# Kernel optimization log

Measured on AMD Instinct MI355X. Metric: run time of the kernel, lower is better.

Reference implementation:

```python
import jax, jax.numpy as jnp
import numpy as np
from jax import lax

B, K, Z, C, H, W = 32, 7, 64, 3, 64, 64
G = H + 6  # decoder grid for 'small' variant
ITERS = 3
SCALE = Z ** -0.5
EPS = 1e-8


def _pe(h, w):
    # matches SlotAttention.create_positional_embedding: shape [w, h, 4]
    ww = jnp.linspace(0.0, 1.0, w)
    hh = jnp.linspace(0.0, 1.0, h)
    a = jnp.broadcast_to((1.0 - ww)[:, None], (w, h))  # dist_right
    b = jnp.broadcast_to(ww[:, None], (w, h))          # dist_left
    c = jnp.broadcast_to(hh[None, :], (w, h))          # dist_top
    d = jnp.broadcast_to((1.0 - hh)[None, :], (w, h))  # dist_bottom
    return jnp.stack([a, b, c, d], -1)


def _ln(x, g, b):
    m = x.mean(-1, keepdims=True)
    v = ((x - m) ** 2).mean(-1, keepdims=True)
    return (x - m) * lax.rsqrt(v + 1e-5) * g + b


def _conv(x, w, b, p):
    y = lax.conv_general_dilated(x, w, (1, 1), [(p, p), (p, p)],
                                 dimension_numbers=('NCHW', 'OIHW', 'NCHW'))
    return y + b[None, :, None, None]


def setup_inputs() -> dict:
    key = jax.random.key(0)
    ks = iter(jax.random.split(key, 64))
    nrm = lambda shape, s=0.05: jax.random.normal(next(ks), shape, jnp.float32) * s
    d = {}
    d['inputs'] = jax.random.normal(next(ks), (B, C, H, W), jnp.float32)
    d['noise'] = jax.random.normal(next(ks), (B * K, Z), jnp.float32)
    d['enc_pos_w'] = nrm((4, 64)); d['enc_pos_b'] = jnp.zeros(64, jnp.float32)
    d['ec1_w'] = nrm((64, 3, 5, 5)); d['ec1_b'] = jnp.zeros(64, jnp.float32)
    d['ec2_w'] = nrm((64, 64, 5, 5)); d['ec2_b'] = jnp.zeros(64, jnp.float32)
    d['ec3_w'] = nrm((64, 64, 5, 5)); d['ec3_b'] = jnp.zeros(64, jnp.float32)
    d['ec4_w'] = nrm((64, 64, 5, 5)); d['ec4_b'] = jnp.zeros(64, jnp.float32)
    d['ln1_g'] = jnp.ones(64, jnp.float32); d['ln1_b'] = jnp.zeros(64, jnp.float32)
    d['fc1_w'] = nrm((64, 64)); d['fc1_b'] = jnp.zeros(64, jnp.float32)
    d['fc2_w'] = nrm((64, 64)); d['fc2_b'] = jnp.zeros(64, jnp.float32)
    d['lns_g'] = jnp.ones(Z, jnp.float32); d['lns_b'] = jnp.zeros(Z, jnp.float32)
    d['lnf_g'] = jnp.ones(Z, jnp.float32); d['lnf_b'] = jnp.zeros(Z, jnp.float32)
    d['q_w'] = nrm((Z, Z)); d['k_w'] = nrm((64, Z)); d['v_w'] = nrm((64, Z))
    d['mlp1_w'] = nrm((Z, 128)); d['mlp1_b'] = jnp.zeros(128, jnp.float32)
    d['mlp2_w'] = nrm((128, Z)); d['mlp2_b'] = jnp.zeros(Z, jnp.float32)
    d['gru_wih'] = nrm((3 * Z, Z)); d['gru_whh'] = nrm((3 * Z, Z))
    d['gru_bih'] = jnp.zeros(3 * Z, jnp.float32); d['gru_bhh'] = jnp.zeros(3 * Z, jnp.float32)
    d['init_slots'] = jnp.concatenate([jnp.zeros((1, Z), jnp.float32), jnp.ones((1, Z), jnp.float32)], 1)
    d['dec_pos_w'] = nrm((4, Z)); d['dec_pos_b'] = jnp.zeros(Z, jnp.float32)
    d['dc1_w'] = nrm((32, Z, 5, 5)); d['dc1_b'] = jnp.zeros(32, jnp.float32)
    d['dc2_w'] = nrm((32, 32, 5, 5)); d['dc2_b'] = jnp.zeros(32, jnp.float32)
    d['dc3_w'] = nrm((32, 32, 5, 5)); d['dc3_b'] = jnp.zeros(32, jnp.float32)
    d['dc4_w'] = nrm((4, 32, 3, 3)); d['dc4_b'] = jnp.zeros(4, jnp.float32)
    return d


def _forward(inputs, noise, enc_pos_w, enc_pos_b, ec1_w, ec1_b, ec2_w, ec2_b,
             ec3_w, ec3_b, ec4_w, ec4_b, ln1_g, ln1_b, fc1_w, fc1_b, fc2_w, fc2_b,
             lns_g, lns_b, lnf_g, lnf_b, q_w, k_w, v_w, mlp1_w, mlp1_b, mlp2_w,
             mlp2_b, gru_wih, gru_whh, gru_bih, gru_bhh, init_slots, dec_pos_w,
             dec_pos_b, dc1_w, dc1_b, dc2_w, dc2_b, dc3_w, dc3_b, dc4_w, dc4_b):
    # ---- encoder ----
    h = jax.nn.relu(_conv(inputs, ec1_w, ec1_b, 2))
    h = jax.nn.relu(_conv(h, ec2_w, ec2_b, 2))
    h = jax.nn.relu(_conv(h, ec3_w, ec3_b, 2))
    h = jax.nn.relu(_conv(h, ec4_w, ec4_b, 2))
    h = h.transpose(0, 2, 3, 1)                        # [B,H,W,64]
    pe = _pe(H, W) @ enc_pos_w + enc_pos_b             # [W,H,64] (H==W)
    h = h + pe[None]
    feat = h.reshape(B, H * W, 64)
    feat = _ln(feat, ln1_g, ln1_b)
    feat = jax.nn.relu(feat @ fc1_w + fc1_b) @ fc2_w + fc2_b
    k = feat @ k_w                                     # [B,N,Z]
    v = feat @ v_w
    # ---- slot init: Normal(loc, softplus(sp)).rsample() ----
    loc, sp = jnp.split(init_slots, 2, axis=1)
    slots = (loc + jax.nn.softplus(sp) * noise).reshape(B, K, Z)
    # ---- iterative slot attention ----
    for _ in range(ITERS):
        prev = slots
        q = (_ln(prev, lns_g, lns_b) @ q_w) * SCALE
        dots = jnp.einsum('bid,bjd->bij', q, k)        # [B,K,N]
        attn = jax.nn.softmax(dots, axis=1) + EPS      # normalize over slots
        attn = attn / attn.sum(-1, keepdims=True)      # renormalize over keys
        updates = jnp.einsum('bjd,bij->bid', v, attn)  # [B,K,Z]
        # GRU cell (single step), torch gate order r,z,n
        gi = updates.reshape(-1, Z) @ gru_wih.T + gru_bih
        gh = prev.reshape(-1, Z) @ gru_whh.T + gru_bhh
        ir, iz, inn = jnp.split(gi, 3, -1)
        hr, hz, hn = jnp.split(gh, 3, -1)
        r = jax.nn.sigmoid(ir + hr)
        zg = jax.nn.sigmoid(iz + hz)
        n = jnp.tanh(inn + r * hn)
        slots = ((1.0 - zg) * n + zg * prev.reshape(-1, Z)).reshape(B, K, Z)
        slots = slots + (jax.nn.relu(_ln(slots, lnf_g, lnf_b) @ mlp1_w + mlp1_b) @ mlp2_w + mlp2_b)
    # ---- spatial-broadcast decoder ('small') ----
    flat = slots.reshape(B * K, Z)
    zb = jnp.broadcast_to(flat[:, :, None, None], (B * K, Z, G, G))
    pe_d = (_pe(G, G) @ dec_pos_w + dec_pos_b).transpose(2, 0, 1)  # [Z,G,G]
    zb = zb + pe_d[None]
    o = jax.nn.relu(_conv(zb, dc1_w, dc1_b, 1))        # 70->68
    o = jax.nn.relu(_conv(o, dc2_w, dc2_b, 1))         # 68->66
    o = jax.nn.relu(_conv(o, dc3_w, dc3_b, 1))         # 66->64
    o = _conv(o, dc4_w, dc4_b, 1)                      # 64->64, 4ch
    x_loc = jax.nn.sigmoid(o[:, :3]).reshape(B, K, C, H, W)
    mask_logits = o[:, 3].reshape(B, K, 1, H, W)
    mask_logp = jax.nn.log_softmax(mask_logits, axis=1)
    x_orig = (inputs + 1.0) / 2.0
    recon = (x_loc * jnp.exp(mask_logp)).sum(1)
    mse = ((x_orig - recon) ** 2).sum() / B
    return mse, x_loc, mask_logp, slots


def reference(inputs, noise, enc_pos_w, enc_pos_b, ec1_w, ec1_b, ec2_w, ec2_b,
              ec3_w, ec3_b, ec4_w, ec4_b, ln1_g, ln1_b, fc1_w, fc1_b, fc2_w, fc2_b,
              lns_g, lns_b, lnf_g, lnf_b, q_w, k_w, v_w, mlp1_w, mlp1_b, mlp2_w,
              mlp2_b, gru_wih, gru_whh, gru_bih, gru_bhh, init_slots, dec_pos_w,
              dec_pos_b, dc1_w, dc1_b, dc2_w, dc2_b, dc3_w, dc3_b, dc4_w, dc4_b):
    return _forward(inputs, noise, enc_pos_w, enc_pos_b, ec1_w, ec1_b, ec2_w, ec2_b,
                    ec3_w, ec3_b, ec4_w, ec4_b, ln1_g, ln1_b, fc1_w, fc1_b, fc2_w, fc2_b,
                    lns_g, lns_b, lnf_g, lnf_b, q_w, k_w, v_w, mlp1_w, mlp1_b, mlp2_w,
                    mlp2_b, gru_wih, gru_whh, gru_bih, gru_bhh, init_slots, dec_pos_w,
                    dec_pos_b, dc1_w, dc1_b, dc2_w, dc2_b, dc3_w, dc3_b, dc4_w, dc4_b)
```

## Files before the change

kernel.cpp:

```cpp
#include <hip/hip_runtime.h>
#include <math.h>

typedef short bf16x8 __attribute__((ext_vector_type(8)));
typedef float f32x4 __attribute__((ext_vector_type(4)));

#define WS_B0   0u
#define WS_B1   4194304u
#define WS_K    8388608u
#define WS_V    16777216u
#define WS_ATTN 25165824u
#define WS_PART 26083328u
#define WS_SLOT 26327040u
#define WS_ROW  26341376u
#define SCALE_ 0.125f

#define OFF_PEB   0u
#define OFF_WCLS  160000u
#define OFF_S     180000u
#define OFF_ZB    250000u

__device__ __forceinline__ float wave_sum(float v) {
#pragma unroll
    for (int m = 32; m >= 1; m >>= 1) v += __shfl_xor(v, m, 64);
    return v;
}
__device__ __forceinline__ unsigned short f2bf(float f) {
    unsigned u = __float_as_uint(f);
    u = u + 0x7fffu + ((u >> 16) & 1u);
    return (unsigned short)(u >> 16);
}
__device__ __forceinline__ float bf2f(unsigned short h) {
    return __uint_as_float(((unsigned)h) << 16);
}

__global__ __launch_bounds__(256) void pack_weights(
    const float* __restrict__ w, unsigned short* __restrict__ wp,
    int CIN, int COUT_STORE, int KS, int NT, int total)
{
    int t = blockIdx.x * 256 + threadIdx.x;
    if (t >= total) return;
    int lane = t & 63;
    int nt = (t >> 6) % NT;
    int ch = t / (64 * NT);
    int CPT = CIN / 32;
    int cic = ch % CPT;
    int tap = ch / CPT;
    int ky = tap / KS, kx = tap % KS;
    int co = nt * 16 + (lane & 15);
    int k0 = cic * 32 + (lane >> 4) * 8;
    unsigned short v[8];
#pragma unroll
    for (int j = 0; j < 8; ++j) {
        int ci = k0 + j;
        float f = (co < COUT_STORE) ? w[((size_t)(co * CIN + ci) * KS + ky) * KS + kx] : 0.f;
        v[j] = f2bf(f);
    }
    *(uint4*)(wp + (size_t)t * 8) = *(uint4*)v;
}

__global__ __launch_bounds__(256) void pack_weights3(
    const float* __restrict__ w0, const float* __restrict__ w1,
    const float* __restrict__ w2, unsigned short* __restrict__ wp)
{
    int t = blockIdx.x * 256 + threadIdx.x;
    if (t >= 38400) return;
    int which = t / 12800;
    int tt = t % 12800;
    const float* w = (which == 0) ? w0 : ((which == 1) ? w1 : w2);
    unsigned short* dst = wp + (size_t)which * 102400;
    int lane = tt & 63;
    int nt = (tt >> 6) & 3;
    int ch = tt >> 8;
    int cic = ch & 1;
    int tap = ch >> 1;
    int ky = tap / 5, kx = tap % 5;
    int co = nt * 16 + (lane & 15);
    int k0 = cic * 32 + (lane >> 4) * 8;
    unsigned short v[8];
#pragma unroll
    for (int j = 0; j < 8; ++j) {
        int ci = k0 + j;
        v[j] = f2bf(w[((size_t)(co * 64 + ci) * 5 + ky) * 5 + kx]);
    }
    *(uint4*)(dst + (size_t)tt * 8) = *(uint4*)v;
}

__global__ __launch_bounds__(256) void pack_fc4(
    const float* __restrict__ w0, const float* __restrict__ w1,
    const float* __restrict__ w2, const float* __restrict__ w3,
    unsigned short* __restrict__ wp)
{
    int t = blockIdx.x * 256 + threadIdx.x;
    if (t >= 2048) return;
    int which = t / 512;
    int tt = t % 512;
    const float* w = (which == 0) ? w0 : ((which == 1) ? w1 : ((which == 2) ? w2 : w3));
    unsigned short* dst = wp + (size_t)which * 4096;
    int lane = tt & 63;
    int nt = (tt >> 6) & 3;
    int ck = tt >> 8;
    int n = nt * 16 + (lane & 15);
    int k0 = ck * 32 + (lane >> 4) * 8;
    unsigned short v[8];
#pragma unroll
    for (int j = 0; j < 8; ++j) v[j] = f2bf(w[(size_t)(k0 + j) * 64 + n]);
    *(uint4*)(dst + (size_t)tt * 8) = *(uint4*)v;
}

template<int CIN, int NTT, int NTU, int KS, int PAD, int NSTORE, int RELU, int OUTF32>
__global__ __launch_bounds__(256) void conv_mfma(
    const unsigned short* __restrict__ in, const unsigned short* __restrict__ wpack,
    const float* __restrict__ bias, void* __restrict__ outv,
    int Hin, int Win, int Hout, int Wout, int tilesX, int tilesY)
{
    constexpr int TS = 16, TH = TS + KS - 1;
    constexpr int CPT = CIN / 32;
    constexpr int G8 = CIN / 8;
    constexpr int CS = NTT / NTU;
    __shared__ __align__(16) unsigned short tile[TH][TH][CIN];
    const int tpb = tilesX * tilesY;
    const int blk = blockIdx.x;
    const int n = blk / (tpb * CS);
    const int rem = blk % (tpb * CS);
    const int t = rem / CS;
    const int cog = rem % CS;
    const int ntb = cog * NTU;
    const int ty0 = (t / tilesX) * TS, tx0 = (t % tilesX) * TS;
    const int tid = threadIdx.x;

    const unsigned short* inb = in + (size_t)n * Hin * Win * CIN;
    for (int idx = tid; idx < TH * TH * G8; idx += 256) {
        const int r = idx / (TH * G8);
        const int p = idx % (TH * G8);
        const int c = p / G8;
        const int chunk = p % G8;
        const int g = (chunk - c) & (G8 - 1);
        int iy = ty0 - PAD + r, ix = tx0 - PAD + c;
        uint4 vv = make_uint4(0, 0, 0, 0);
        if (iy >= 0 && iy < Hin && ix >= 0 && ix < Win)
            vv = *(const uint4*)(inb + ((size_t)iy * Win + ix) * CIN + g * 8);
        *(uint4*)&tile[r][c][chunk * 8] = vv;
    }
    __syncthreads();

    const int wv = tid >> 6, lane = tid & 63;
    const int q = lane >> 4, m = lane & 15;
    const int row0 = wv * 4;
    f32x4 acc[4][NTU];
#pragma unroll
    for (int mt = 0; mt < 4; ++mt)
#pragma unroll
        for (int nt = 0; nt < NTU; ++nt) acc[mt][nt] = (f32x4){0.f, 0.f, 0.f, 0.f};

#pragma unroll
    for (int cic = 0; cic < CPT; ++cic) {
#pragma unroll
        for (int kx = 0; kx < KS; ++kx) {
            bf16x8 B[KS][NTU];
#pragma unroll
            for (int ky = 0; ky < KS; ++ky)
#pragma unroll
                for (int nt = 0; nt < NTU; ++nt)
                    B[ky][nt] = *(const bf16x8*)(wpack +
                        ((size_t)(((ky * KS + kx) * CPT + cic) * NTT + ntb + nt) * 64 + lane) * 8);
            const int cbase = m + kx;
            const int slot = (cic * 32 + q * 8 + cbase * 8) % CIN;
#pragma unroll
            for (int ir = 0; ir < KS + 3; ++ir) {
                bf16x8 afr = *(const bf16x8*)&tile[row0 + ir][cbase][slot];
#pragma unroll
                for (int ky = 0; ky < KS; ++ky) {
                    const int mt = ir - ky;
                    if (mt < 0 || mt > 3) continue;
#pragma unroll
                    for (int nt = 0; nt < NTU; ++nt)
                        acc[mt][nt] = __builtin_amdgcn_mfma_f32_16x16x32_bf16(afr, B[ky][nt], acc[mt][nt], 0, 0, 0);
                }
            }
        }
    }

#pragma unroll
    for (int nt = 0; nt < NTU; ++nt) {
        const int co = (ntb + nt) * 16 + m;
        const float bv = (co < NSTORE) ? bias[co] : 0.f;
#pragma unroll
        for (int mt = 0; mt < 4; ++mt) {
            const int oy = ty0 + wv * 4 + mt;
#pragma unroll
            for (int j = 0; j < 4; ++j) {
                const int ox = tx0 + q * 4 + j;
                if (oy < Hout && ox < Wout && co < NSTORE) {
                    float v = acc[mt][nt][j] + bv;
                    if (RELU) v = fmaxf(v, 0.f);
                    size_t o = (((size_t)n * Hout + oy) * Wout + ox) * NSTORE + co;
                    if (OUTF32) ((float*)outv)[o] = v;
                    else ((unsigned short*)outv)[o] = f2bf(v);
                }
            }
        }
    }
}

__global__ __launch_bounds__(256) void pe_synth(
    const float* __restrict__ dpw, const float* __restrict__ dpb,
    unsigned short* __restrict__ peb, float* __restrict__ zbias)
{
    const int tid = threadIdx.x;
    if (blockIdx.x == 0 && tid < 32) zbias[tid] = 0.f;
    const int pix = blockIdx.x * 256 + tid;
    if (pix >= 4900) return;
    const int iy = pix / 70, ix = pix % 70;
    const float fy = iy * (1.f / 69.f), fx = ix * (1.f / 69.f);
    unsigned short v[64];
#pragma unroll
    for (int ci = 0; ci < 64; ++ci) {
        float p = (1.f - fy) * dpw[ci] + fy * dpw[64 + ci]
                + fx * dpw[128 + ci] + (1.f - fx) * dpw[192 + ci] + dpb[ci];
        v[ci] = f2bf(p);
    }
    uint4* ob = (uint4*)(peb + (size_t)pix * 64);
#pragma unroll
    for (int i = 0; i < 8; ++i) ob[i] = ((uint4*)v)[i];
}

__global__ __launch_bounds__(256) void wcls_build(
    const float* __restrict__ w, float* __restrict__ wcls)
{
    int idx = blockIdx.x * 256 + threadIdx.x;
    if (idx >= 9 * 32 * 64) return;
    int cls = idx / (32 * 64);
    int co = (idx / 64) % 32;
    int ci = idx % 64;
    int rc = cls / 3, cc = cls % 3;
    int ky0 = (rc == 0) ? 1 : 0, ky1 = (rc == 2) ? 3 : 4;
    int kx0 = (cc == 0) ? 1 : 0, kx1 = (cc == 2) ? 3 : 4;
    float s = 0.f;
    const float* wb = w + (size_t)(co * 64 + ci) * 25;
    for (int ky = ky0; ky <= ky1; ++ky)
        for (int kx = kx0; kx <= kx1; ++kx)
            s += wb[ky * 5 + kx];
    wcls[idx] = s;
}

__global__ __launch_bounds__(256) void slot_s(
    const float* __restrict__ slots, const float* __restrict__ wcls,
    float* __restrict__ S)
{
    int idx = blockIdx.x * 256 + threadIdx.x;
    if (idx >= 224 * 9 * 32) return;
    int n = idx / (9 * 32);
    int cls = (idx / 32) % 9;
    int co = idx % 32;
    const float* sl = slots + n * 64;
    const float* wc = wcls + (size_t)(cls * 32 + co) * 64;
    float s = 0.f;
#pragma unroll
    for (int ci = 0; ci < 64; ++ci) s = fmaf(sl[ci], wc[ci], s);
    S[idx] = s;
}

__global__ __launch_bounds__(256) void dc1_assemble(
    const float* __restrict__ P, const float* __restrict__ S,
    const float* __restrict__ bias, int n0,
    unsigned short* __restrict__ out)
{
    const int gid = blockIdx.x * 256 + threadIdx.x;
    const int nl = gid / 4624;
    const int pix = gid % 4624;
    const int oy = pix / 68, ox = pix % 68;
    const int rc = (oy == 0) ? 0 : ((oy == 67) ? 2 : 1);
    const int cc = (ox == 0) ? 0 : ((ox == 67) ? 2 : 1);
    const float* Sp = S + ((size_t)(n0 + nl) * 9 + (rc * 3 + cc)) * 32;
    const float* Pp = P + (size_t)pix * 32;
    unsigned short v[32];
#pragma unroll
    for (int co = 0; co < 32; ++co)
        v[co] = f2bf(fmaxf(bias[co] + Pp[co] + Sp[co], 0.f));
    uint4* ob = (uint4*)(out + ((size_t)nl * 4624 + pix) * 32);
#pragma unroll
    for (int i = 0; i < 4; ++i) ob[i] = ((uint4*)v)[i];
}

__global__ __launch_bounds__(256) void conv_ec1(
    const float* __restrict__ in, const float* __restrict__ wts,
    const float* __restrict__ bias, unsigned short* __restrict__ out)
{
    __shared__ float tile[3][20][21];
    const int blk = blockIdx.x;
    const int n = blk >> 6;
    const int sub = blk & 63;
    const int t = sub >> 2;
    const int cog = sub & 3;
    const int ty0 = (t >> 2) * 16, tx0 = (t & 3) * 16;
    const int tid = threadIdx.x;
    for (int idx = tid; idx < 1200; idx += 256) {
        int ci = idx / 400, rc = idx % 400;
        int r = rc / 20, c = rc % 20;
        int gy = ty0 + r - 2, gx = tx0 + c - 2;
        float v = 0.f;
        if (gy >= 0 && gy < 64 && gx >= 0 && gx < 64)
            v = in[((size_t)n * 3 + ci) * 4096 + gy * 64 + gx];
        tile[ci][r][c] = v;
    }
    __syncthreads();
    const int lx = tid & 15, ly = tid >> 4;
    float acc[16];
#pragma unroll
    for (int co = 0; co < 16; ++co) acc[co] = bias[cog * 16 + co];
    for (int ci = 0; ci < 3; ++ci) {
        float val[25];
#pragma unroll
        for (int ky = 0; ky < 5; ++ky)
#pragma unroll
            for (int kx = 0; kx < 5; ++kx) val[ky * 5 + kx] = tile[ci][ly + ky][lx + kx];
#pragma unroll
        for (int co = 0; co < 16; ++co) {
            const float* wc = wts + (size_t)((cog * 16 + co) * 3 + ci) * 25;
            float a = acc[co];
#pragma unroll
            for (int tt = 0; tt < 25; ++tt) a = fmaf(val[tt], wc[tt], a);
            acc[co] = a;
        }
    }
    unsigned short tmp[16];
#pragma unroll
    for (int co = 0; co < 16; ++co) tmp[co] = f2bf(fmaxf(acc[co], 0.f));
    uint4* ob = (uint4*)(out + (((size_t)n * 64 + ty0 + ly) * 64 + tx0 + lx) * 64 + cog * 16);
    ob[0] = ((uint4*)tmp)[0];
    ob[1] = ((uint4*)tmp)[1];
}

__global__ __launch_bounds__(256) void encoder_tail_mfma(
    const unsigned short* __restrict__ h4,
    const float* __restrict__ epw, const float* __restrict__ epb,
    const float* __restrict__ ln1g, const float* __restrict__ ln1b,
    const unsigned short* __restrict__ pfc1, const float* __restrict__ fc1b,
    const unsigned short* __restrict__ pfc2, const float* __restrict__ fc2b,
    const unsigned short* __restrict__ pkw, const unsigned short* __restrict__ pvw,
    unsigned short* __restrict__ kout, unsigned short* __restrict__ vout)
{
    __shared__ __align__(16) unsigned short X[64][72];
    const int b = blockIdx.x >> 6;
    const int y = blockIdx.x & 63;
    const int tid = threadIdx.x;

    {
        const int p = tid >> 2, sub = tid & 3;
        const unsigned short* hp = h4 + ((((size_t)b * 64 + y) * 64 + p) * 64) + sub * 16;
        unsigned short raw[16];
        *(uint4*)(raw)     = *(const uint4*)hp;
        *(uint4*)(raw + 8) = *(const uint4*)(hp + 8);
        const float fy = y * (1.f / 63.f), fx = p * (1.f / 63.f);
        float f[16];
        float s1 = 0.f, s2 = 0.f;
#pragma unroll
        for (int j = 0; j < 16; ++j) {
            int ch = sub * 16 + j;
            float pe = (1.f - fy) * epw[ch] + fy * epw[64 + ch]
                     + fx * epw[128 + ch] + (1.f - fx) * epw[192 + ch] + epb[ch];
            float v = bf2f(raw[j]) + pe;
            f[j] = v;
            s1 += v;
            s2 += v * v;
        }
        s1 += __shfl_xor(s1, 1, 64); s1 += __shfl_xor(s1, 2, 64);
        s2 += __shfl_xor(s2, 1, 64); s2 += __shfl_xor(s2, 2, 64);
        const float m = s1 * (1.f / 64.f);
        const float var = s2 * (1.f / 64.f) - m * m;
        const float inv = rsqrtf(var + 1e-5f);
        unsigned short xb[16];
#pragma unroll
        for (int j = 0; j < 16; ++j) {
            int ch = sub * 16 + j;
            xb[j] = f2bf((f[j] - m) * inv * ln1g[ch] + ln1b[ch]);
        }
        *(uint4*)&X[p][sub * 16]     = ((uint4*)xb)[0];
        *(uint4*)&X[p][sub * 16 + 8] = ((uint4*)xb)[1];
    }
    __syncthreads();

    const int w = tid >> 6, lane = tid & 63;
    const int q = lane >> 4, m_ = lane & 15;
    const int row0 = w * 16;

    {
        f32x4 a1[4];
#pragma unroll
        for (int nt = 0; nt < 4; ++nt) a1[nt] = (f32x4){0.f, 0.f, 0.f, 0.f};
#pragma unroll
        for (int ck = 0; ck < 2; ++ck) {
            bf16x8 afr = *(const bf16x8*)&X[row0 + m_][ck * 32 + q * 8];
#pragma unroll
            for (int nt = 0; nt < 4; ++nt) {
                bf16x8 bfr = *(const bf16x8*)(pfc1 + ((size_t)((ck * 4 + nt) * 64 + lane)) * 8);
                a1[nt] = __builtin_amdgcn_mfma_f32_16x16x32_bf16(afr, bfr, a1[nt], 0, 0, 0);
            }
        }
        __syncthreads();
#pragma unroll
        for (int nt = 0; nt < 4; ++nt) {
            const float bb = fc1b[nt * 16 + m_];
#pragma unroll
            for (int reg = 0; reg < 4; ++reg)
                X[row0 + q * 4 + reg][nt * 16 + m_] = f2bf(fmaxf(a1[nt][reg] + bb, 0.f));
        }
    }
    __syncthreads();

    {
        f32x4 a2[4];
#pragma unroll
        for (int nt = 0; nt < 4; ++nt) a2[nt] = (f32x4){0.f, 0.f, 0.f, 0.f};
#pragma unroll
        for (int ck = 0; ck < 2; ++ck) {
            bf16x8 afr = *(const bf16x8*)&X[row0 + m_][ck * 32 + q * 8];
#pragma unroll
            for (int nt = 0; nt < 4; ++nt) {
                bf16x8 bfr = *(const bf16x8*)(pfc2 + ((size_t)((ck * 4 + nt) * 64 + lane)) * 8);
                a2[nt] = __builtin_amdgcn_mfma_f32_16x16x32_bf16(afr, bfr, a2[nt], 0, 0, 0);
            }
        }
        __syncthreads();
#pragma unroll
        for (int nt = 0; nt < 4; ++nt) {
            const float bb = fc2b[nt * 16 + m_];
#pragma unroll
            for (int reg = 0; reg < 4; ++reg)
                X[row0 + q * 4 + reg][nt * 16 + m_] = f2bf(a2[nt][reg] + bb);
        }
    }
    __syncthreads();

    {
        f32x4 ak[4], av[4];
#pragma unroll
        for (int nt = 0; nt < 4; ++nt) {
            ak[nt] = (f32x4){0.f, 0.f, 0.f, 0.f};
            av[nt] = (f32x4){0.f, 0.f, 0.f, 0.f};
        }
#pragma unroll
        for (int ck = 0; ck < 2; ++ck) {
            bf16x8 afr = *(const bf16x8*)&X[row0 + m_][ck * 32 + q * 8];
#pragma unroll
            for (int nt = 0; nt < 4; ++nt) {
                bf16x8 bk = *(const bf16x8*)(pkw + ((size_t)((ck * 4 + nt) * 64 + lane)) * 8);
                bf16x8 bv = *(const bf16x8*)(pvw + ((size_t)((ck * 4 + nt) * 64 + lane)) * 8);
                ak[nt] = __builtin_amdgcn_mfma_f32_16x16x32_bf16(afr, bk, ak[nt], 0, 0, 0);
                av[nt] = __builtin_amdgcn_mfma_f32_16x16x32_bf16(afr, bv, av[nt], 0, 0, 0);
            }
        }
        const size_t base = ((size_t)b * 4096) + y * 64 + row0;
#pragma unroll
        for (int nt = 0; nt < 4; ++nt) {
            const int ch = nt * 16 + m_;
#pragma unroll
            for (int reg = 0; reg < 4; ++reg) {
                const size_t o = (base + q * 4 + reg) * 64 + ch;
                kout[o] = f2bf(ak[nt][reg]);
                vout[o] = f2bf(av[nt][reg]);
            }
        }
    }
}

__global__ __launch_bounds__(256) void slot_init(
    const float* __restrict__ noise, const float* __restrict__ init_slots,
    float* __restrict__ slots, float* __restrict__ rowsum)
{
    int i = blockIdx.x * 256 + threadIdx.x;
    if (i < 224) rowsum[i] = 0.f;
    if (i < 224 * 64) {
        int z = i & 63;
        float spl = log1pf(expf(init_slots[64 + z]));
        slots[i] = init_slots[z] + spl * noise[i];
    }
}

__global__ __launch_bounds__(256) void attn_fused(
    const unsigned short* __restrict__ kbuf, const unsigned short* __restrict__ vbuf,
    const float* __restrict__ slots,
    const float* __restrict__ lnsg, const float* __restrict__ lnsb,
    const float* __restrict__ qw,
    float* __restrict__ part, float* __restrict__ rowsum)
{
    __shared__ float qs[7][64];
    __shared__ float ash[256][7];
    __shared__ float red7[7][4];
    __shared__ float redv[4][7][64];
    const int b = blockIdx.x >> 4;
    const int js = blockIdx.x & 15;
    const int j0 = js * 256;
    const int tid = threadIdx.x;
    const int lane = tid & 63, wv = tid >> 6;

    for (int i = wv; i < 7; i += 4) {
        float s = slots[(b * 7 + i) * 64 + lane];
        float m = wave_sum(s) * (1.f / 64.f);
        float d = s - m;
        float var = wave_sum(d * d) * (1.f / 64.f);
        float x = d * rsqrtf(var + 1e-5f) * lnsg[lane] + lnsb[lane];
        float qv = 0.f;
        for (int c = 0; c < 64; ++c) qv = fmaf(__shfl(x, c, 64), qw[c * 64 + lane], qv);
        qs[i][lane] = qv * SCALE_;
    }
    __syncthreads();

    {
        const int j = j0 + tid;
        float kr[64];
        const unsigned short* kp = kbuf + (((size_t)b * 4096) + j) * 64;
#pragma unroll
        for (int d8 = 0; d8 < 8; ++d8) {
            uint4 kv = ((const uint4*)kp)[d8];
            const unsigned short* h = (const unsigned short*)&kv;
#pragma unroll
            for (int z = 0; z < 8; ++z) kr[d8 * 8 + z] = bf2f(h[z]);
        }
        float dots[7];
#pragma unroll
        for (int i = 0; i < 7; ++i) {
            float a = 0.f;
#pragma unroll
            for (int d = 0; d < 64; ++d) a = fmaf(kr[d], qs[i][d], a);
            dots[i] = a;
        }
        float mx = dots[0];
#pragma unroll
        for (int i = 1; i < 7; ++i) mx = fmaxf(mx, dots[i]);
        float sum = 0.f;
#pragma unroll
        for (int i = 0; i < 7; ++i) { dots[i] = expf(dots[i] - mx); sum += dots[i]; }
        const float inv = 1.f / sum;
#pragma unroll
        for (int i = 0; i < 7; ++i) {
            float a = dots[i] * inv + 1e-8f;
            dots[i] = a;
            ash[tid][i] = a;
        }
#pragma unroll
        for (int i = 0; i < 7; ++i) {
            float s = wave_sum(dots[i]);
            if (lane == 0) red7[i][wv] = s;
        }
    }
    __syncthreads();
    if (tid < 7)
        atomicAdd(&rowsum[b * 7 + tid], red7[tid][0] + red7[tid][1] + red7[tid][2] + red7[tid][3]);

    {
        const int d = lane, jc = wv;
        float acc[7];
#pragma unroll
        for (int i = 0; i < 7; ++i) acc[i] = 0.f;
        for (int jl = jc; jl < 256; jl += 4) {
            float av = bf2f(vbuf[(((size_t)b * 4096) + j0 + jl) * 64 + d]);
#pragma unroll
            for (int i = 0; i < 7; ++i)
                acc[i] = fmaf(ash[jl][i], av, acc[i]);
        }
#pragma unroll
        for (int i = 0; i < 7; ++i) redv[jc][i][d] = acc[i];
    }
    __syncthreads();
    if (tid < 7 * 64) {
        int i = tid / 64, dd = tid % 64;
        float s = redv[0][i][dd] + redv[1][i][dd] + redv[2][i][dd] + redv[3][i][dd];
        part[((((size_t)b * 16) + js) * 7 + i) * 64 + dd] = s;
    }
}

__global__ __launch_bounds__(64) void gru_mlp(
    float* __restrict__ slots, const float* __restrict__ part,
    float* __restrict__ rowsum,
    const float* __restrict__ wih, const float* __restrict__ whh,
    const float* __restrict__ bih, const float* __restrict__ bhh,
    const float* __restrict__ lnfg, const float* __restrict__ lnfb,
    const float* __restrict__ m1w, const float* __restrict__ m1b,
    const float* __restrict__ m2w, const float* __restrict__ m2b)
{
    const int n = blockIdx.x;
    const int b = n / 7, i = n % 7;
    const int l = threadIdx.x;
    float upd = 0.f;
    for (int js = 0; js < 16; ++js)
        upd += part[((((size_t)b * 16) + js) * 7 + i) * 64 + l];
    upd /= rowsum[n];
    if (l == 0) rowsum[n] = 0.f;
    const float prev = slots[n * 64 + l];
    float gi0 = bih[l], gi1 = bih[64 + l], gi2 = bih[128 + l];
    float gh0 = bhh[l], gh1 = bhh[64 + l], gh2 = bhh[128 + l];
    for (int c = 0; c < 64; ++c) {
        float u = __shfl(upd, c, 64), p = __shfl(prev, c, 64);
        gi0 = fmaf(u, wih[l * 64 + c], gi0);
        gi1 = fmaf(u, wih[(64 + l) * 64 + c], gi1);
        gi2 = fmaf(u, wih[(128 + l) * 64 + c], gi2);
        gh0 = fmaf(p, whh[l * 64 + c], gh0);
        gh1 = fmaf(p, whh[(64 + l) * 64 + c], gh1);
        gh2 = fmaf(p, whh[(128 + l) * 64 + c], gh2);
    }
    float r  = 1.f / (1.f + expf(-(gi0 + gh0)));
    float zg = 1.f / (1.f + expf(-(gi1 + gh1)));
    float nn = tanhf(gi2 + r * gh2);
    float s = (1.f - zg) * nn + zg * prev;
    float m = wave_sum(s) * (1.f / 64.f);
    float d = s - m;
    float var = wave_sum(d * d) * (1.f / 64.f);
    float x = d * rsqrtf(var + 1e-5f) * lnfg[l] + lnfb[l];
    float h0 = m1b[l], h1 = m1b[64 + l];
    for (int c = 0; c < 64; ++c) {
        float xv = __shfl(x, c, 64);
        h0 = fmaf(xv, m1w[c * 128 + l], h0);
        h1 = fmaf(xv, m1w[c * 128 + 64 + l], h1);
    }
    h0 = fmaxf(h0, 0.f); h1 = fmaxf(h1, 0.f);
    float o = m2b[l];
    for (int c = 0; c < 64; ++c) {
        o = fmaf(__shfl(h0, c, 64), m2w[c * 64 + l], o);
        o = fmaf(__shfl(h1, c, 64), m2w[(64 + c) * 64 + l], o);
    }
    slots[n * 64 + l] = s + o;
}

__global__ __launch_bounds__(256) void finalize_k(
    const float* __restrict__ dc4out, const float* __restrict__ inputs,
    float* __restrict__ out)
{
    const int tid = threadIdx.x;
    const int gp = blockIdx.x * 256 + tid;
    const int b = gp >> 12, p = gp & 4095;
    float4 o4[7];
#pragma unroll
    for (int k = 0; k < 7; ++k)
        o4[k] = ((const float4*)dc4out)[(size_t)(b * 7 + k) * 4096 + p];
    float mx = o4[0].w;
#pragma unroll
    for (int k = 1; k < 7; ++k) mx = fmaxf(mx, o4[k].w);
    float s = 0.f;
#pragma unroll
    for (int k = 0; k < 7; ++k) s += expf(o4[k].w - mx);
    const float lse = mx + logf(s);
    float recon0 = 0.f, recon1 = 0.f, recon2 = 0.f;
    float* xl = out + 1;
    float* ml = out + 2752513;
#pragma unroll
    for (int k = 0; k < 7; ++k) {
        float lp = o4[k].w - lse;
        ml[((size_t)(b * 7 + k)) * 4096 + p] = lp;
        float w = expf(lp);
        float x0 = 1.f / (1.f + expf(-o4[k].x));
        float x1 = 1.f / (1.f + expf(-o4[k].y));
        float x2 = 1.f / (1.f + expf(-o4[k].z));
        xl[(((size_t)(b * 7 + k)) * 3 + 0) * 4096 + p] = x0;
        xl[(((size_t)(b * 7 + k)) * 3 + 1) * 4096 + p] = x1;
        xl[(((size_t)(b * 7 + k)) * 3 + 2) * 4096 + p] = x2;
        recon0 = fmaf(x0, w, recon0);
        recon1 = fmaf(x1, w, recon1);
        recon2 = fmaf(x2, w, recon2);
    }
    float err = 0.f;
    {
        float xo = (inputs[((size_t)b * 3 + 0) * 4096 + p] + 1.f) * 0.5f;
        float dd = xo - recon0; err += dd * dd;
        xo = (inputs[((size_t)b * 3 + 1) * 4096 + p] + 1.f) * 0.5f;
        dd = xo - recon1; err += dd * dd;
        xo = (inputs[((size_t)b * 3 + 2) * 4096 + p] + 1.f) * 0.5f;
        dd = xo - recon2; err += dd * dd;
    }
    float wsum = wave_sum(err);
    __shared__ float red[4];
    const int lane = tid & 63, wv = tid >> 6;
    if (lane == 0) red[wv] = wsum;
    __syncthreads();
    if (tid == 0) atomicAdd(out, (red[0] + red[1] + red[2] + red[3]) * (1.f / 32.f));
}

__global__ __launch_bounds__(256) void copy_slots(const float* __restrict__ slots,
                                                  float* __restrict__ out)
{
    int i = blockIdx.x * 256 + threadIdx.x;
    if (i == 0) out[0] = 0.f;
    if (i < 14336) out[3670017 + i] = slots[i];
}

extern "C" void kernel_launch(void* const* d_in, const int* in_sizes, int n_in,
                              void* d_out, int out_size, void* d_ws, size_t ws_size,
                              hipStream_t stream) {
    (void)in_sizes; (void)n_in; (void)out_size; (void)ws_size;
    const float* inputs = (const float*)d_in[0];
    const float* noise  = (const float*)d_in[1];
    const float* epw  = (const float*)d_in[2];
    const float* epb  = (const float*)d_in[3];
    const float* ec1w = (const float*)d_in[4];
    const float* ec1b = (const float*)d_in[5];
    const float* ec2w = (const float*)d_in[6];
    const float* ec2b = (const float*)d_in[7];
    const float* ec3w = (const float*)d_in[8];
    const float* ec3b = (const float*)d_in[9];
    const float* ec4w = (const float*)d_in[10];
    const float* ec4b = (const float*)d_in[11];
    const float* ln1g = (const float*)d_in[12];
    const float* ln1b = (const float*)d_in[13];
    const float* fc1w = (const float*)d_in[14];
    const float* fc1b = (const float*)d_in[15];
    const float* fc2w = (const float*)d_in[16];
    const float* fc2b = (const float*)d_in[17];
    const float* lnsg = (const float*)d_in[18];
    const float* lnsb = (const float*)d_in[19];
    const float* lnfg = (const float*)d_in[20];
    const float* lnfb = (const float*)d_in[21];
    const float* qw   = (const float*)d_in[22];
    const float* kw   = (const float*)d_in[23];
    const float* vw   = (const float*)d_in[24];
    const float* m1w  = (const float*)d_in[25];
    const float* m1b  = (const float*)d_in[26];
    const float* m2w  = (const float*)d_in[27];
    const float* m2b  = (const float*)d_in[28];
    const float* wih  = (const float*)d_in[29];
    const float* whh  = (const float*)d_in[30];
    const float* bih  = (const float*)d_in[31];
    const float* bhh  = (const float*)d_in[32];
    const float* init_slots = (const float*)d_in[33];
    const float* dpw  = (const float*)d_in[34];
    const float* dpb  = (const float*)d_in[35];
    const float* dc1w = (const float*)d_in[36];
    const float* dc1b = (const float*)d_in[37];
    const float* dc2w = (const float*)d_in[38];
    const float* dc2b = (const float*)d_in[39];
    const float* dc3w = (const float*)d_in[40];
    const float* dc3b = (const float*)d_in[41];
    const float* dc4w = (const float*)d_in[42];
    const float* dc4b = (const float*)d_in[43];

    float* ws = (float*)d_ws;
    unsigned short* B0 = (unsigned short*)(ws + WS_B0);
    unsigned short* B1 = (unsigned short*)(ws + WS_B1);
    unsigned short* K = (unsigned short*)(ws + WS_K);
    unsigned short* V = (unsigned short*)(ws + WS_V);
    unsigned short* dping = (unsigned short*)(ws + WS_B0);
    unsigned short* dpong = (unsigned short*)(ws + WS_K);
    float* dc4out = ws + WS_V;
    unsigned short* PK = (unsigned short*)(ws + WS_V + 4194304u);
    unsigned short* p_ec2 = PK, *p_ec3 = PK + 102400, *p_ec4 = PK + 204800;
    unsigned short* p_dc1 = PK, *p_dc2 = PK + 51200, *p_dc3 = PK + 76800, *p_dc4 = PK + 102400;
    float* attn  = ws + WS_ATTN;
    unsigned short* PFC = (unsigned short*)attn;
    unsigned short* p_fc1 = PFC, *p_fc2 = PFC + 4096, *p_kw = PFC + 8192, *p_vw = PFC + 12288;
    unsigned short* peb = (unsigned short*)(attn + OFF_PEB);
    float* wclsb = attn + OFF_WCLS;
    float* Sbuf  = attn + OFF_S;
    float* zbias = attn + OFF_ZB;
    float* part  = ws + WS_PART;
    float* P     = ws + WS_PART;
    float* slots = ws + WS_SLOT;
    float* rowsum = ws + WS_ROW;
    float* out = (float*)d_out;

    pack_weights3<<<150, 256, 0, stream>>>(ec2w, ec3w, ec4w, p_ec2);
    pack_fc4<<<8, 256, 0, stream>>>(fc1w, fc2w, kw, vw, p_fc1);

    conv_ec1<<<2048, 256, 0, stream>>>(inputs, ec1w, ec1b, B0);
    conv_mfma<64, 4, 2, 5, 2, 64, 1, 0><<<1024, 256, 0, stream>>>(B0, p_ec2, ec2b, B1, 64, 64, 64, 64, 4, 4);
    conv_mfma<64, 4, 2, 5, 2, 64, 1, 0><<<1024, 256, 0, stream>>>(B1, p_ec3, ec3b, B0, 64, 64, 64, 64, 4, 4);
    conv_mfma<64, 4, 2, 5, 2, 64, 1, 0><<<1024, 256, 0, stream>>>(B0, p_ec4, ec4b, B1, 64, 64, 64, 64, 4, 4);
    encoder_tail_mfma<<<2048, 256, 0, stream>>>(B1, epw, epb, ln1g, ln1b,
                                                p_fc1, fc1b, p_fc2, fc2b, p_kw, p_vw, K, V);
    slot_init<<<56, 256, 0, stream>>>(noise, init_slots, slots, rowsum);

    for (int it = 0; it < 3; ++it) {
        attn_fused<<<512, 256, 0, stream>>>(K, V, slots, lnsg, lnsb, qw, part, rowsum);
        gru_mlp<<<224, 64, 0, stream>>>(slots, part, rowsum, wih, whh, bih, bhh,
                                        lnfg, lnfb, m1w, m1b, m2w, m2b);
    }

    pack_weights<<<25, 256, 0, stream>>>(dc1w, p_dc1, 64, 32, 5, 2, 6400);
    pack_weights<<<13, 256, 0, stream>>>(dc2w, p_dc2, 32, 32, 5, 2, 3200);
    pack_weights<<<13, 256, 0, stream>>>(dc3w, p_dc3, 32, 32, 5, 2, 3200);
    pack_weights<<<3, 256, 0, stream>>>(dc4w, p_dc4, 32, 4, 3, 1, 576);
    pe_synth<<<20, 256, 0, stream>>>(dpw, dpb, peb, zbias);
    conv_mfma<64, 2, 2, 5, 1, 32, 0, 1><<<25, 256, 0, stream>>>(peb, p_dc1, zbias, P, 70, 70, 68, 68, 5, 5);
    wcls_build<<<72, 256, 0, stream>>>(dc1w, wclsb);
    slot_s<<<252, 256, 0, stream>>>(slots, wclsb, Sbuf);

    for (int ch = 0; ch < 2; ++ch) {
        float* d4o = dc4out + (size_t)ch * 112 * 4 * 4096;
        dc1_assemble<<<2023, 256, 0, stream>>>(P, Sbuf, dc1b, ch * 112, dping);
        conv_mfma<32, 2, 2, 5, 1, 32, 1, 0><<<2800, 256, 0, stream>>>(dping, p_dc2, dc2b, dpong, 68, 68, 66, 66, 5, 5);
        conv_mfma<32, 2, 2, 5, 1, 32, 1, 0><<<1792, 256, 0, stream>>>(dpong, p_dc3, dc3b, dping, 66, 66, 64, 64, 4, 4);
        conv_mfma<32, 1, 1, 3, 1, 4, 0, 1><<<1792, 256, 0, stream>>>(dping, p_dc4, dc4b, d4o, 64, 64, 64, 64, 4, 4);
    }

    copy_slots<<<56, 256, 0, stream>>>(slots, out);
    finalize_k<<<512, 256, 0, stream>>>(dc4out, inputs, out);
}
```

Measured before the change: 771.3 us.

## Replace LDS-tiled conv with register-direct MFMA conv reading global memory

```diff
diff --git a/kernel.cpp b/kernel.cpp
--- a/kernel.cpp
+++ b/kernel.cpp
@@ -10,6 +10,7 @@
 #define WS_V    16777216u
 #define WS_ATTN 25165824u
 #define WS_PART 26083328u
+#define WS_ZP   26312704u
 #define WS_SLOT 26327040u
 #define WS_ROW  26341376u
 #define SCALE_ 0.125f
@@ -60,8 +61,10 @@
 
 __global__ __launch_bounds__(256) void pack_weights3(
     const float* __restrict__ w0, const float* __restrict__ w1,
-    const float* __restrict__ w2, unsigned short* __restrict__ wp)
-{
+    const float* __restrict__ w2, unsigned short* __restrict__ wp,
+    float* __restrict__ zpage)
+{
+    if (blockIdx.x == 0 && threadIdx.x < 64) zpage[threadIdx.x] = 0.f;
     int t = blockIdx.x * 256 + threadIdx.x;
     if (t >= 38400) return;
     int which = t / 12800;
@@ -105,6 +108,108 @@
 #pragma unroll
     for (int j = 0; j < 8; ++j) v[j] = f2bf(w[(size_t)(k0 + j) * 64 + n]);
     *(uint4*)(dst + (size_t)tt * 8) = *(uint4*)v;
+}
+
+template<int CIN, int NTT, int KS, int PAD, int NSTORE, int RELU, int OUTF32, int GPW>
+__global__ __launch_bounds__(256) void conv_reg(
+    const unsigned short* __restrict__ in, const unsigned short* __restrict__ wpack,
+    const float* __restrict__ bias, void* __restrict__ outv,
+    const unsigned short* __restrict__ zpage,
+    int Hin, int Win, int Hout, int Wout,
+    int gx_count, int groups_per_img, int total_groups)
+{
+    constexpr int CPT = CIN / 32;
+    const int tid = threadIdx.x;
+    const int lane = tid & 63;
+    const int wv = tid >> 6;
+    const int q = lane >> 4, m = lane & 15;
+    const int pr = m >> 3, pc = m & 7;
+
+    const int g0 = (blockIdx.x * 4 + wv) * GPW;
+
+    int imgg[GPW], oyg[GPW], oxg[GPW];
+    unsigned masky[GPW], maskx[GPW];
+    const unsigned short* pbase[GPW];
+    bool gv[GPW];
+#pragma unroll
+    for (int g = 0; g < GPW; ++g) {
+        int gi = g0 + g;
+        gv[g] = gi < total_groups;
+        int gic = gv[g] ? gi : 0;
+        int n = gic / groups_per_img;
+        int r = gic % groups_per_img;
+        int band = r / gx_count;
+        int gx = r % gx_count;
+        imgg[g] = n;
+        oyg[g] = band * 2;
+        oxg[g] = gx * 8;
+        const int iyb = oyg[g] + pr - PAD;
+        const int ixb = oxg[g] + pc - PAD;
+        unsigned my = 0, mx = 0;
+#pragma unroll
+        for (int k = 0; k < KS; ++k) {
+            my |= ((unsigned)(iyb + k) < (unsigned)Hin) ? (1u << k) : 0u;
+            mx |= ((unsigned)(ixb + k) < (unsigned)Win) ? (1u << k) : 0u;
+        }
+        masky[g] = gv[g] ? my : 0u;
+        maskx[g] = mx;
+        pbase[g] = in + ((long long)((n * Hin + iyb) * Win + ixb)) * CIN;
+    }
+
+    f32x4 acc[GPW][NTT];
+#pragma unroll
+    for (int g = 0; g < GPW; ++g)
+#pragma unroll
+        for (int nt = 0; nt < NTT; ++nt) acc[g][nt] = (f32x4){0.f, 0.f, 0.f, 0.f};
+
+    for (int cic = 0; cic < CPT; ++cic) {
+        const int ch_off = cic * 32 + q * 8;
+#pragma unroll
+        for (int ky = 0; ky < KS; ++ky) {
+#pragma unroll
+            for (int kx = 0; kx < KS; ++kx) {
+                const int tap = ky * KS + kx;
+                bf16x8 B[NTT];
+#pragma unroll
+                for (int nt = 0; nt < NTT; ++nt)
+                    B[nt] = *(const bf16x8*)(wpack +
+                        ((size_t)((tap * CPT + cic) * NTT + nt) * 64 + lane) * 8);
+                const int toff = (ky * Win + kx) * CIN + ch_off;
+#pragma unroll
+                for (int g = 0; g < GPW; ++g) {
+                    const bool v = (((masky[g] >> ky) & (maskx[g] >> kx)) & 1u) != 0u;
+                    const unsigned short* ap = v ? (pbase[g] + toff) : zpage;
+                    bf16x8 a = *(const bf16x8*)ap;
+#pragma unroll
+                    for (int nt = 0; nt < NTT; ++nt)
+                        acc[g][nt] = __builtin_amdgcn_mfma_f32_16x16x32_bf16(a, B[nt], acc[g][nt], 0, 0, 0);
+                }
+            }
+        }
+    }
+
+#pragma unroll
+    for (int g = 0; g < GPW; ++g) {
+        if (!gv[g]) continue;
+#pragma unroll
+        for (int nt = 0; nt < NTT; ++nt) {
+            const int co = nt * 16 + m;
+            const float bv = (co < NSTORE) ? bias[co] : 0.f;
+#pragma unroll
+            for (int j = 0; j < 4; ++j) {
+                const int p = q * 4 + j;
+                const int oy = oyg[g] + (p >> 3);
+                const int ox = oxg[g] + (p & 7);
+                if (ox < Wout && co < NSTORE) {
+                    float vv = acc[g][nt][j] + bv;
+                    if (RELU) vv = fmaxf(vv, 0.f);
+                    size_t o = (((size_t)imgg[g] * Hout + oy) * Wout + ox) * NSTORE + co;
+                    if (OUTF32) ((float*)outv)[o] = vv;
+                    else ((unsigned short*)outv)[o] = f2bf(vv);
+                }
+            }
+        }
+    }
 }
 
 template<int CIN, int NTT, int NTU, int KS, int PAD, int NSTORE, int RELU, int OUTF32>
@@ -752,17 +857,19 @@
     float* zbias = attn + OFF_ZB;
     float* part  = ws + WS_PART;
     float* P     = ws + WS_PART;
+    float* zpage = ws + WS_ZP;
     float* slots = ws + WS_SLOT;
     float* rowsum = ws + WS_ROW;
     float* out = (float*)d_out;
-
-    pack_weights3<<<150, 256, 0, stream>>>(ec2w, ec3w, ec4w, p_ec2);
+    const unsigned short* zp16 = (const unsigned short*)zpage;
+
+    pack_weights3<<<150, 256, 0, stream>>>(ec2w, ec3w, ec4w, p_ec2, zpage);
     pack_fc4<<<8, 256, 0, stream>>>(fc1w, fc2w, kw, vw, p_fc1);
 
     conv_ec1<<<2048, 256, 0, stream>>>(inputs, ec1w, ec1b, B0);
-    conv_mfma<64, 4, 2, 5, 2, 64, 1, 0><<<1024, 256, 0, stream>>>(B0, p_ec2, ec2b, B1, 64, 64, 64, 64, 4, 4);
-    conv_mfma<64, 4, 2, 5, 2, 64, 1, 0><<<1024, 256, 0, stream>>>(B1, p_ec3, ec3b, B0, 64, 64, 64, 64, 4, 4);
-    conv_mfma<64, 4, 2, 5, 2, 64, 1, 0><<<1024, 256, 0, stream>>>(B0, p_ec4, ec4b, B1, 64, 64, 64, 64, 4, 4);
+    conv_reg<64, 4, 5, 2, 64, 1, 0, 2><<<1024, 256, 0, stream>>>(B0, p_ec2, ec2b, B1, zp16, 64, 64, 64, 64, 8, 256, 8192);
+    conv_reg<64, 4, 5, 2, 64, 1, 0, 2><<<1024, 256, 0, stream>>>(B1, p_ec3, ec3b, B0, zp16, 64, 64, 64, 64, 8, 256, 8192);
+    conv_reg<64, 4, 5, 2, 64, 1, 0, 2><<<1024, 256, 0, stream>>>(B0, p_ec4, ec4b, B1, zp16, 64, 64, 64, 64, 8, 256, 8192);
     encoder_tail_mfma<<<2048, 256, 0, stream>>>(B1, epw, epb, ln1g, ln1b,
                                                 p_fc1, fc1b, p_fc2, fc2b, p_kw, p_vw, K, V);
     slot_init<<<56, 256, 0, stream>>>(noise, init_slots, slots, rowsum);
@@ -785,9 +892,9 @@
     for (int ch = 0; ch < 2; ++ch) {
         float* d4o = dc4out + (size_t)ch * 112 * 4 * 4096;
         dc1_assemble<<<2023, 256, 0, stream>>>(P, Sbuf, dc1b, ch * 112, dping);
-        conv_mfma<32, 2, 2, 5, 1, 32, 1, 0><<<2800, 256, 0, stream>>>(dping, p_dc2, dc2b, dpong, 68, 68, 66, 66, 5, 5);
-        conv_mfma<32, 2, 2, 5, 1, 32, 1, 0><<<1792, 256, 0, stream>>>(dpong, p_dc3, dc3b, dping, 66, 66, 64, 64, 4, 4);
-        conv_mfma<32, 1, 1, 3, 1, 4, 0, 1><<<1792, 256, 0, stream>>>(dping, p_dc4, dc4b, d4o, 64, 64, 64, 64, 4, 4);
+        conv_reg<32, 2, 5, 1, 32, 1, 0, 4><<<2079, 256, 0, stream>>>(dping, p_dc2, dc2b, dpong, zp16, 68, 68, 66, 66, 9, 297, 33264);
+        conv_reg<32, 2, 5, 1, 32, 1, 0, 4><<<1792, 256, 0, stream>>>(dpong, p_dc3, dc3b, dping, zp16, 66, 66, 64, 64, 8, 256, 28672);
+        conv_reg<32, 1, 3, 1, 4, 0, 1, 8><<<896, 256, 0, stream>>>(dping, p_dc4, dc4b, d4o, zp16, 64, 64, 64, 64, 8, 256, 28672);
     }
 
     copy_slots<<<56, 256, 0, stream>>>(slots, out);
```

After: 1.117 ms. 1.45x slower.

## Load conv input tiles directly to LDS and widen encoder conv output per block

Applied to the files above, without the earlier changes.

```diff
diff --git a/kernel.cpp b/kernel.cpp
--- a/kernel.cpp
+++ b/kernel.cpp
@@ -10,6 +10,7 @@
 #define WS_V    16777216u
 #define WS_ATTN 25165824u
 #define WS_PART 26083328u
+#define WS_ZP   26312704u
 #define WS_SLOT 26327040u
 #define WS_ROW  26341376u
 #define SCALE_ 0.125f
@@ -31,6 +32,12 @@
 }
 __device__ __forceinline__ float bf2f(unsigned short h) {
     return __uint_as_float(((unsigned)h) << 16);
+}
+__device__ __forceinline__ void gl_lds16(const void* src, void* lds_base) {
+    __builtin_amdgcn_global_load_lds(
+        (const __attribute__((address_space(1))) unsigned int*)src,
+        (__attribute__((address_space(3))) unsigned int*)lds_base,
+        16, 0, 0);
 }
 
 __global__ __launch_bounds__(256) void pack_weights(
@@ -60,8 +67,10 @@
 
 __global__ __launch_bounds__(256) void pack_weights3(
     const float* __restrict__ w0, const float* __restrict__ w1,
-    const float* __restrict__ w2, unsigned short* __restrict__ wp)
-{
+    const float* __restrict__ w2, unsigned short* __restrict__ wp,
+    float* __restrict__ zpage)
+{
+    if (blockIdx.x == 0 && threadIdx.x < 64) zpage[threadIdx.x] = 0.f;
     int t = blockIdx.x * 256 + threadIdx.x;
     if (t >= 38400) return;
     int which = t / 12800;
@@ -111,13 +120,16 @@
 __global__ __launch_bounds__(256) void conv_mfma(
     const unsigned short* __restrict__ in, const unsigned short* __restrict__ wpack,
     const float* __restrict__ bias, void* __restrict__ outv,
+    const unsigned short* __restrict__ zpage,
     int Hin, int Win, int Hout, int Wout, int tilesX, int tilesY)
 {
     constexpr int TS = 16, TH = TS + KS - 1;
     constexpr int CPT = CIN / 32;
     constexpr int G8 = CIN / 8;
     constexpr int CS = NTT / NTU;
-    __shared__ __align__(16) unsigned short tile[TH][TH][CIN];
+    constexpr int TOTCH = TH * TH * G8;
+    constexpr int TOTCH_PAD = (TOTCH + 63) & ~63;
+    __shared__ __align__(16) unsigned short tile[TOTCH_PAD * 8];
     const int tpb = tilesX * tilesY;
     const int blk = blockIdx.x;
     const int n = blk / (tpb * CS);
@@ -127,23 +139,23 @@
     const int ntb = cog * NTU;
     const int ty0 = (t / tilesX) * TS, tx0 = (t % tilesX) * TS;
     const int tid = threadIdx.x;
+    const int wv = tid >> 6, lane = tid & 63;
 
     const unsigned short* inb = in + (size_t)n * Hin * Win * CIN;
-    for (int idx = tid; idx < TH * TH * G8; idx += 256) {
+    for (int cb = wv * 64; cb < TOTCH; cb += 256) {
+        const int idx = cb + lane;
         const int r = idx / (TH * G8);
         const int p = idx % (TH * G8);
         const int c = p / G8;
         const int chunk = p % G8;
         const int g = (chunk - c) & (G8 - 1);
-        int iy = ty0 - PAD + r, ix = tx0 - PAD + c;
-        uint4 vv = make_uint4(0, 0, 0, 0);
-        if (iy >= 0 && iy < Hin && ix >= 0 && ix < Win)
-            vv = *(const uint4*)(inb + ((size_t)iy * Win + ix) * CIN + g * 8);
-        *(uint4*)&tile[r][c][chunk * 8] = vv;
+        const int iy = ty0 - PAD + r, ix = tx0 - PAD + c;
+        const bool ok = (idx < TOTCH) && ((unsigned)iy < (unsigned)Hin) && ((unsigned)ix < (unsigned)Win);
+        const unsigned short* src = ok ? (inb + ((size_t)iy * Win + ix) * CIN + g * 8) : zpage;
+        gl_lds16(src, tile + (size_t)cb * 8);
     }
     __syncthreads();
 
-    const int wv = tid >> 6, lane = tid & 63;
     const int q = lane >> 4, m = lane & 15;
     const int row0 = wv * 4;
     f32x4 acc[4][NTU];
@@ -167,7 +179,7 @@
             const int slot = (cic * 32 + q * 8 + cbase * 8) % CIN;
 #pragma unroll
             for (int ir = 0; ir < KS + 3; ++ir) {
-                bf16x8 afr = *(const bf16x8*)&tile[row0 + ir][cbase][slot];
+                bf16x8 afr = *(const bf16x8*)&tile[((row0 + ir) * TH + cbase) * CIN + slot];
 #pragma unroll
                 for (int ky = 0; ky < KS; ++ky) {
                     const int mt = ir - ky;
@@ -752,17 +764,19 @@
     float* zbias = attn + OFF_ZB;
     float* part  = ws + WS_PART;
     float* P     = ws + WS_PART;
+    float* zpage = ws + WS_ZP;
     float* slots = ws + WS_SLOT;
     float* rowsum = ws + WS_ROW;
     float* out = (float*)d_out;
-
-    pack_weights3<<<150, 256, 0, stream>>>(ec2w, ec3w, ec4w, p_ec2);
+    const unsigned short* zp16 = (const unsigned short*)zpage;
+
+    pack_weights3<<<150, 256, 0, stream>>>(ec2w, ec3w, ec4w, p_ec2, zpage);
     pack_fc4<<<8, 256, 0, stream>>>(fc1w, fc2w, kw, vw, p_fc1);
 
     conv_ec1<<<2048, 256, 0, stream>>>(inputs, ec1w, ec1b, B0);
-    conv_mfma<64, 4, 2, 5, 2, 64, 1, 0><<<1024, 256, 0, stream>>>(B0, p_ec2, ec2b, B1, 64, 64, 64, 64, 4, 4);
-    conv_mfma<64, 4, 2, 5, 2, 64, 1, 0><<<1024, 256, 0, stream>>>(B1, p_ec3, ec3b, B0, 64, 64, 64, 64, 4, 4);
-    conv_mfma<64, 4, 2, 5, 2, 64, 1, 0><<<1024, 256, 0, stream>>>(B0, p_ec4, ec4b, B1, 64, 64, 64, 64, 4, 4);
+    conv_mfma<64, 4, 4, 5, 2, 64, 1, 0><<<512, 256, 0, stream>>>(B0, p_ec2, ec2b, B1, zp16, 64, 64, 64, 64, 4, 4);
+    conv_mfma<64, 4, 4, 5, 2, 64, 1, 0><<<512, 256, 0, stream>>>(B1, p_ec3, ec3b, B0, zp16, 64, 64, 64, 64, 4, 4);
+    conv_mfma<64, 4, 4, 5, 2, 64, 1, 0><<<512, 256, 0, stream>>>(B0, p_ec4, ec4b, B1, zp16, 64, 64, 64, 64, 4, 4);
     encoder_tail_mfma<<<2048, 256, 0, stream>>>(B1, epw, epb, ln1g, ln1b,
                                                 p_fc1, fc1b, p_fc2, fc2b, p_kw, p_vw, K, V);
     slot_init<<<56, 256, 0, stream>>>(noise, init_slots, slots, rowsum);
@@ -778,16 +792,16 @@
     pack_weights<<<13, 256, 0, stream>>>(dc3w, p_dc3, 32, 32, 5, 2, 3200);
     pack_weights<<<3, 256, 0, stream>>>(dc4w, p_dc4, 32, 4, 3, 1, 576);
     pe_synth<<<20, 256, 0, stream>>>(dpw, dpb, peb, zbias);
-    conv_mfma<64, 2, 2, 5, 1, 32, 0, 1><<<25, 256, 0, stream>>>(peb, p_dc1, zbias, P, 70, 70, 68, 68, 5, 5);
+    conv_mfma<64, 2, 2, 5, 1, 32, 0, 1><<<25, 256, 0, stream>>>(peb, p_dc1, zbias, P, zp16, 70, 70, 68, 68, 5, 5);
     wcls_build<<<72, 256, 0, stream>>>(dc1w, wclsb);
     slot_s<<<252, 256, 0, stream>>>(slots, wclsb, Sbuf);
 
     for (int ch = 0; ch < 2; ++ch) {
         float* d4o = dc4out + (size_t)ch * 112 * 4 * 4096;
         dc1_assemble<<<2023, 256, 0, stream>>>(P, Sbuf, dc1b, ch * 112, dping);
-        conv_mfma<32, 2, 2, 5, 1, 32, 1, 0><<<2800, 256, 0, stream>>>(dping, p_dc2, dc2b, dpong, 68, 68, 66, 66, 5, 5);
-        conv_mfma<32, 2, 2, 5, 1, 32, 1, 0><<<1792, 256, 0, stream>>>(dpong, p_dc3, dc3b, dping, 66, 66, 64, 64, 4, 4);
-        conv_mfma<32, 1, 1, 3, 1, 4, 0, 1><<<1792, 256, 0, stream>>>(dping, p_dc4, dc4b, d4o, 64, 64, 64, 64, 4, 4);
+        conv_mfma<32, 2, 2, 5, 1, 32, 1, 0><<<2800, 256, 0, stream>>>(dping, p_dc2, dc2b, dpong, zp16, 68, 68, 66, 66, 5, 5);
+        conv_mfma<32, 2, 2, 5, 1, 32, 1, 0><<<1792, 256, 0, stream>>>(dpong, p_dc3, dc3b, dping, zp16, 66, 66, 64, 64, 4, 4);
+        conv_mfma<32, 1, 1, 3, 1, 4, 0, 1><<<1792, 256, 0, stream>>>(dping, p_dc4, dc4b, d4o, zp16, 64, 64, 64, 64, 4, 4);
     }
 
     copy_slots<<<56, 256, 0, stream>>>(slots, out);
```

Measured after the change: 741.0 us. 3.9% less time.
